# Kernel optimization log

Measured on AMD Instinct MI355X. Metric: run time of the kernel, lower is better.

The kernel has to match this reference:

```python
import jax, jax.numpy as jnp
import numpy as np

B, T, I, H, C, L = 64, 256, 256, 1024, 1000, 2


def setup_inputs() -> dict:
    key = jax.random.key(0)
    ks = jax.random.split(key, 10)
    stdv = 1.0 / np.sqrt(H)
    u = lambda k, shape: jax.random.uniform(k, shape, jnp.float32, -stdv, stdv)
    return {
        "x": jax.random.normal(ks[0], (B, T, I), jnp.float32),
        # gate order: g (tanh), i, f, o — stacked on leading axis
        "W0x": u(ks[1], (4, I, H)),
        "W0h": u(ks[2], (4, H, H)),
        "b0": u(ks[3], (4, H)),
        "W1x": u(ks[4], (4, H, H)),
        "W1h": u(ks[5], (4, H, H)),
        "b1": u(ks[6], (4, H)),
        "Wo": u(ks[7], (H, C)),
        "bo": u(ks[8], (C,)),
    }


def _cell(x, h, c, Wx, Wh, b):
    # z: [4, B, H] — one fused contraction for the 4 gates
    z = jnp.einsum('bi,gih->gbh', x, Wx) + jnp.einsum('bh,ghk->gbk', h, Wh) + b[:, None, :]
    g = jnp.tanh(z[0])
    i = jax.nn.sigmoid(z[1])
    f = jax.nn.sigmoid(z[2])
    o = jax.nn.sigmoid(z[3])
    c_new = g * i + c * f
    h_new = jnp.tanh(c_new) * o
    return h_new, c_new


def reference(x, W0x, W0h, b0, W1x, W1h, b1, Wo, bo):
    xt = jnp.transpose(x, (1, 0, 2))  # [T, B, I] like x.permute(1,0,2)
    zeros = jnp.zeros((B, H), x.dtype)
    init = (zeros, zeros, zeros, zeros)  # h0, c0, h1, c1

    def step(carry, x_t):
        h0, c0, h1, c1 = carry
        h0, c0 = _cell(x_t, h0, c0, W0x, W0h, b0)
        h1, c1 = _cell(h0, h1, c1, W1x, W1h, b1)
        return (h0, c0, h1, c1), None

    (h0, c0, h1, c1), _ = jax.lax.scan(step, init, xt)
    return jnp.matmul(h1, Wo) + bo
```

## Files before the change

kernel.cpp:

```cpp
#include <hip/hip_runtime.h>
#include <cstddef>

#define B_  64
#define T_  256
#define I_  256
#define H_  1024
#define C_  1000
#define BH_ (B_ * H_)
#define SLOTS_B_ 24

typedef _Float16 f16;
typedef __attribute__((ext_vector_type(8))) _Float16 f16x8;
typedef __attribute__((ext_vector_type(4))) float f32x4;

__device__ __forceinline__ float sigmoid_(float v) { return 1.0f / (1.0f + __expf(-v)); }
__device__ __forceinline__ float tanh_(float v) {
  float e = __expf(-2.0f * fabsf(v));
  float t = (1.0f - e) / (1.0f + e);
  return copysignf(t, v);
}

__device__ __forceinline__ void storeH2(f16* p, float a, float b) {
  union { f16 h[2]; unsigned u; } pk;
  pk.h[0] = (f16)a; pk.h[1] = (f16)b;
  __hip_atomic_store((unsigned*)p, pk.u, __ATOMIC_RELAXED, __HIP_MEMORY_SCOPE_AGENT);
}


__device__ __forceinline__ unsigned ldS(unsigned* p) {
  return __hip_atomic_load(p, __ATOMIC_RELAXED, __HIP_MEMORY_SCOPE_AGENT);
}

__device__ __forceinline__ void waitRel(unsigned* a, unsigned ta,
                                        unsigned* b, unsigned tb) {
  int g = 0;
  for (;;) {
    unsigned va = ldS(a);
    unsigned vb = ldS(b);
    if (va >= ta && vb >= tb) break;
    __builtin_amdgcn_s_sleep(1);
    if (++g > (1 << 17)) break;
  }
}

template<bool IS_L1>
__device__ __forceinline__ void role_main(
    const f16* __restrict__ x16,
    const float* __restrict__ Wx, const float* __restrict__ Wh,
    const float* __restrict__ bias,
    f16* __restrict__ h0hist, f16* __restrict__ h1hist,
    unsigned* sync, int bid, int nslots, int fmask, int lagD,
    float* zbAll, float* cLDS, float* biasLDS)
{
  constexpr int KTOT = IS_L1 ? 64 : 40;
  constexpr int NKT  = KTOT / 4;
  constexpr int KX   = IS_L1 ? 1024 : 256;

  const int tid  = threadIdx.x;
  const int wv   = tid >> 6;
  const int nh   = wv >> 2;
  const int kq   = wv & 3;
  const int lane = tid & 63;
  const int c16  = lane & 15;
  const int quad = lane >> 4;
  const int rr7  = bid & 127;
  const int mgroup  = rr7 & 1;
  const int ubase   = (rr7 >> 1) * 16;
  const int rowbase = mgroup * 32;

  const int  grp       = bid & 7;
  const bool leaderBlk = IS_L1 ? (bid == 128) : (bid == 0);
  unsigned* arrBase = sync + (IS_L1 ?  8 :  0) * 32;
  unsigned* relBase = sync + (IS_L1 ? 24 : 16) * 32;
  unsigned* arrMine = arrBase + grp * 32;
  unsigned* relOwn  = relBase + grp * 32;
  unsigned* relOth  = sync + (IS_L1 ? 16 : 24) * 32 + grp * 32;

  if (tid < 64) biasLDS[tid] = bias[(size_t)(tid >> 4) * H_ + ubase + (tid & 15)];
  cLDS[tid] = 0.0f;

  f16x8 Wreg[2][NKT];
  {
    f16* zpan = (f16*)zbAll + wv * 1024;
#pragma unroll
    for (int ii = 0; ii < NKT; ++ii) {
      const int kt = kq * NKT + ii;
#pragma unroll
      for (int rw = 0; rw < 16; ++rw) {
        const int krow  = rw * 2 + (lane >> 5);
        const int col32 = lane & 31;
        const int g = nh * 2 + (col32 >> 4);
        const int u = col32 & 15;
        const int k = kt * 32 + krow;
        float wval = (k < KX) ? Wx[((size_t)g * KX + k) * H_ + ubase + u]
                              : Wh[((size_t)g * H_ + (k - KX)) * H_ + ubase + u];
        zpan[krow * 32 + col32] = (f16)wval;
      }
#pragma unroll
      for (int nt = 0; nt < 2; ++nt) {
        f16x8 f;
#pragma unroll
        for (int j = 0; j < 8; ++j)
          f[j] = zpan[(quad * 8 + j) * 32 + nt * 16 + c16];
        Wreg[nt][ii] = f;
      }
    }
  }
  __syncthreads();

  const int ktbase = kq * NKT;
  const int row0 = rowbase + c16;

#pragma unroll 1
  for (int p = 0; p <= T_; ++p) {
    const bool active = IS_L1 ? (p >= 1) : (p < T_);
    const int do_fence = (nslots == 2) ? 1
                        : ((fmask < 0) ? 0 : (((p & fmask) == fmask) ? 1 : 0));

    if (tid == 0) {
      unsigned  tb = 0u;
      unsigned* bp = relOwn;
      if (IS_L1) {
        if (active) { bp = relOth; tb = (unsigned)p; }
      } else if (active && lagD >= 0 && p > lagD) {
        bp = relOth; tb = (unsigned)(p - lagD);
      }
      waitRel(relOwn, (unsigned)p, bp, tb);
      if (do_fence) __builtin_amdgcn_fence(__ATOMIC_ACQUIRE, "agent");
    }
    __syncthreads();

    if (active) {
      const int sp  = p % nslots;
      const int spm = (p - 1 + nslots) % nslots;
      const int spp = (p + 1) % nslots;
      const f16* __restrict__ hA = h0hist + (size_t)sp * BH_;
      const f16* __restrict__ hB = h1hist + (size_t)spm * BH_;
      f16* __restrict__ hdst = IS_L1 ? (h1hist + (size_t)sp  * BH_)
                                     : (h0hist + (size_t)spp * BH_);

      f16x8 Abuf[6][2];
      auto loadA = [&](int ii, int slot) {
        const int kt = ktbase + ii;
        const int k  = kt * 32 + quad * 8;
#pragma unroll
        for (int mt2 = 0; mt2 < 2; ++mt2) {
          const int row = row0 + mt2 * 16;
          if (!IS_L1 && k < 256) {
            Abuf[slot][mt2] = *(const f16x8*)(x16 + ((size_t)row * T_ + p) * I_ + k);
          } else if (IS_L1 && k >= 1024) {
            Abuf[slot][mt2] = *(const f16x8*)(hB + (size_t)row * H_ + (k - 1024));
          } else {
            const int kk = IS_L1 ? k : (k - 256);
            Abuf[slot][mt2] = *(const f16x8*)(hA + (size_t)row * H_ + kk);
          }
        }
      };

      f32x4 acc[2][2];
#pragma unroll
      for (int mt2 = 0; mt2 < 2; ++mt2)
#pragma unroll
        for (int nt = 0; nt < 2; ++nt)
          acc[mt2][nt] = (f32x4)0.0f;

      loadA(0, 0); loadA(1, 1); loadA(2, 2);
      loadA(3, 3); loadA(4, 4); loadA(5, 5);
#pragma unroll
      for (int i = 0; i < NKT; ++i) {
        const int sl = i % 6;
        const f16x8 a0 = Abuf[sl][0];
        const f16x8 a1 = Abuf[sl][1];
        if (i + 6 < NKT) loadA(i + 6, (i + 6) % 6);
        acc[0][0] = __builtin_amdgcn_mfma_f32_16x16x32_f16(a0, Wreg[0][i], acc[0][0], 0, 0, 0);
        acc[0][1] = __builtin_amdgcn_mfma_f32_16x16x32_f16(a0, Wreg[1][i], acc[0][1], 0, 0, 0);
        acc[1][0] = __builtin_amdgcn_mfma_f32_16x16x32_f16(a1, Wreg[0][i], acc[1][0], 0, 0, 0);
        acc[1][1] = __builtin_amdgcn_mfma_f32_16x16x32_f16(a1, Wreg[1][i], acc[1][1], 0, 0, 0);
      }

      float* zw = zbAll + (nh * 4 + kq) * 1024;
#pragma unroll
      for (int mt2 = 0; mt2 < 2; ++mt2)
#pragma unroll
        for (int nt = 0; nt < 2; ++nt)
#pragma unroll
          for (int e = 0; e < 4; ++e)
            zw[(mt2 * 2 + nt) * 256 + (quad * 4 + e) * 16 + c16] = acc[mt2][nt][e];

      __syncthreads();

      {
        const int base = tid * 4;
        const int nh1  = base >> 10;
        const int off  = base & 1023;
        f32x4 s = (f32x4)0.0f;
#pragma unroll
        for (int q = 0; q < 4; ++q)
          s += *(const f32x4*)(zbAll + nh1 * 4096 + q * 1024 + off);
        const int nt1 = (off >> 8) & 1;
        const int c0  = off & 15;
        s += *(const f32x4*)(biasLDS + (nh1 * 2 + nt1) * 16 + c0);
        *(f32x4*)(zbAll + nh1 * 4096 + off) = s;
      }
      __syncthreads();

      {
        const int row = tid >> 4, u = tid & 15;
        const int mt2 = row >> 4, r16 = row & 15;
        const float z0 = zbAll[0 * 4096 + (mt2 * 2 + 0) * 256 + r16 * 16 + u];
        const float z1 = zbAll[0 * 4096 + (mt2 * 2 + 1) * 256 + r16 * 16 + u];
        const float z2 = zbAll[1 * 4096 + (mt2 * 2 + 0) * 256 + r16 * 16 + u];
        const float z3 = zbAll[1 * 4096 + (mt2 * 2 + 1) * 256 + r16 * 16 + u];
        const float cv = cLDS[tid];
        const float gt = tanh_(z0);
        const float iv = sigmoid_(z1);
        const float fv = sigmoid_(z2);
        const float ov = sigmoid_(z3);
        const float cn = gt * iv + cv * fv;
        cLDS[tid] = cn;
        const float hn = tanh_(cn) * ov;
        const float hn_hi = __shfl_down(hn, 1);
        if ((tid & 1) == 0)
          storeH2(hdst + (size_t)(rowbase + row) * H_ + ubase + u, hn, hn_hi);
      }
    }

    __syncthreads();
    if (tid == 0) {
      __hip_atomic_fetch_add(arrMine, 1u, __ATOMIC_RELAXED, __HIP_MEMORY_SCOPE_AGENT);
      if (leaderBlk) {
        const unsigned tgt = 16u * (unsigned)(p + 1);
        int gg = 0;
        for (;;) {
          unsigned mn = 0xffffffffu;
#pragma unroll
          for (int j = 0; j < 8; ++j) {
            unsigned v = ldS(arrBase + j * 32);
            mn = (v < mn) ? v : mn;
          }
          if (mn >= tgt) break;
          __builtin_amdgcn_s_sleep(1);
          if (++gg > (1 << 17)) break;
        }
#pragma unroll
        for (int j = 0; j < 8; ++j)
          __hip_atomic_store(relBase + j * 32, (unsigned)(p + 1),
                             __ATOMIC_RELAXED, __HIP_MEMORY_SCOPE_AGENT);
      }
    }
  }
}

__global__ __launch_bounds__(512, 2)
void lstm_persistent(const f16* __restrict__ x16,
                     const float* __restrict__ W0x, const float* __restrict__ W0h, const float* __restrict__ b0,
                     const float* __restrict__ W1x, const float* __restrict__ W1h, const float* __restrict__ b1,
                     f16* h0hist, f16* h1hist, unsigned* sync,
                     int nslots, int fmask, int lagD)
{
  __shared__ float zbAll[8192];
  __shared__ float cLDS[512];
  __shared__ float biasLDS[64];
  const int bid = blockIdx.x;
  if (bid >= 128)
    role_main<true >(x16, W1x, W1h, b1, h0hist, h1hist, sync, bid, nslots, fmask, lagD, zbAll, cLDS, biasLDS);
  else
    role_main<false>(x16, W0x, W0h, b0, h0hist, h1hist, sync, bid, nslots, fmask, lagD, zbAll, cLDS, biasLDS);
}

__global__ void cvt_x(const float* __restrict__ xin, f16* __restrict__ xo)
{
  const int i = (blockIdx.x * 256 + threadIdx.x) * 8;
  const float4 a = *(const float4*)(xin + i);
  const float4 b = *(const float4*)(xin + i + 4);
  f16x8 v;
  v[0] = (f16)a.x; v[1] = (f16)a.y; v[2] = (f16)a.z; v[3] = (f16)a.w;
  v[4] = (f16)b.x; v[5] = (f16)b.y; v[6] = (f16)b.z; v[7] = (f16)b.w;
  *(f16x8*)(xo + i) = v;
}

__global__ void out_gemm(const f16* __restrict__ h1,
                         const float* __restrict__ Wo, const float* __restrict__ bo,
                         float* __restrict__ out)
{
  __shared__ float ht[1024][8];
  const int tid = threadIdx.x;
  const int b0r = blockIdx.y * 4;
  for (int i = tid; i < 4096; i += 128) {
    const int rr = i >> 10, k = i & 1023;
    ht[k][rr] = (float)h1[(size_t)(b0r + rr) * H_ + k];
  }
  __syncthreads();
  const int c = blockIdx.x * 125 + tid;
  if (tid < 125) {
    float a0 = 0.f, a1 = 0.f, a2 = 0.f, a3 = 0.f;
#pragma unroll 4
    for (int k = 0; k < 1024; ++k) {
      const float w = Wo[(size_t)k * C_ + c];
      a0 += ht[k][0] * w;
      a1 += ht[k][1] * w;
      a2 += ht[k][2] * w;
      a3 += ht[k][3] * w;
    }
    const float bb = bo[c];
    out[(size_t)(b0r + 0) * C_ + c] = a0 + bb;
    out[(size_t)(b0r + 1) * C_ + c] = a1 + bb;
    out[(size_t)(b0r + 2) * C_ + c] = a2 + bb;
    out[(size_t)(b0r + 3) * C_ + c] = a3 + bb;
  }
}

extern "C" void kernel_launch(void* const* d_in, const int* in_sizes, int n_in,
                              void* d_out, int out_size, void* d_ws, size_t ws_size,
                              hipStream_t stream)
{
  const float* x   = (const float*)d_in[0];
  const float* W0x = (const float*)d_in[1];
  const float* W0h = (const float*)d_in[2];
  const float* b0  = (const float*)d_in[3];
  const float* W1x = (const float*)d_in[4];
  const float* W1h = (const float*)d_in[5];
  const float* b1  = (const float*)d_in[6];
  const float* Wo  = (const float*)d_in[7];
  const float* bo  = (const float*)d_in[8];

  const size_t slotB = (size_t)BH_ * sizeof(f16);
  const size_t xB    = (size_t)B_ * T_ * I_ * sizeof(f16);
  const size_t needA = 4096 + (size_t)2 * (T_ + 1) * slotB + xB;
  const size_t needB = 4096 + (size_t)2 * SLOTS_B_ * slotB + xB;
  int nslots, fmask, lagD;
  if (ws_size >= needA)      { nslots = T_ + 1;   fmask = -1; lagD = -1; }
  else if (ws_size >= needB) { nslots = SLOTS_B_; fmask = 15; lagD = 7;  }
  else                       { nslots = 2;        fmask = 0;  lagD = 0;  }
  const size_t histB = (size_t)nslots * slotB;

  unsigned* sync  = (unsigned*)d_ws;
  f16* h0hist = (f16*)((char*)d_ws + 4096);
  f16* h1hist = (f16*)((char*)h0hist + histB);
  f16* x16    = (f16*)((char*)h1hist + histB);

  hipMemsetAsync(d_ws, 0, 4096 + slotB, stream);
  hipMemsetAsync(h1hist, 0, slotB, stream);

  hipLaunchKernelGGL(cvt_x, dim3((B_ * T_ * I_) / (256 * 8)), dim3(256), 0, stream, x, x16);

  hipLaunchKernelGGL(lstm_persistent, dim3(256), dim3(512), 0, stream,
                     x16, W0x, W0h, b0, W1x, W1h, b1, h0hist, h1hist, sync,
                     nslots, fmask, lagD);

  f16* h1fin = h1hist + (size_t)(T_ % nslots) * BH_;
  hipLaunchKernelGGL(out_gemm, dim3(8, 16), dim3(128), 0, stream,
                     h1fin, Wo, bo, (float*)d_out);
}
```

Measured before the change: 2.980 ms.

## Replace leader-based barrier with per-batch-half counters and overlap waits with x/h compute

Drops the two-stage arrive/leader/release barrier. Each block now polls eight distributed arrival counters directly, partitioned by layer and batch half (mgroup), so it waits only on the blocks that produce the rows it reads. The K-tiles are remapped so each wave has independent work before each wait: layer 0 computes its x-projection tiles and layer 1 its h0 tiles before waiting on the other dependency. This aims to cut barrier latency and hide part of it behind MFMA work. In exchange, every block spins on eight counters, which adds polling traffic, and correctness now depends on the new counter-slot and indexing scheme.

```diff
diff --git a/kernel.cpp b/kernel.cpp
--- a/kernel.cpp
+++ b/kernel.cpp
@@ -31,13 +31,16 @@
   return __hip_atomic_load(p, __ATOMIC_RELAXED, __HIP_MEMORY_SCOPE_AGENT);
 }
 
-__device__ __forceinline__ void waitRel(unsigned* a, unsigned ta,
-                                        unsigned* b, unsigned tb) {
+__device__ __forceinline__ void waitCtr8(unsigned* base, unsigned tgt) {
   int g = 0;
   for (;;) {
-    unsigned va = ldS(a);
-    unsigned vb = ldS(b);
-    if (va >= ta && vb >= tb) break;
+    unsigned mn = 0xffffffffu;
+#pragma unroll
+    for (int j = 0; j < 8; ++j) {
+      unsigned v = ldS(base + j * 32);
+      mn = (v < mn) ? v : mn;
+    }
+    if (mn >= tgt) break;
     __builtin_amdgcn_s_sleep(1);
     if (++g > (1 << 17)) break;
   }
@@ -52,9 +55,8 @@
     unsigned* sync, int bid, int nslots, int fmask, int lagD,
     float* zbAll, float* cLDS, float* biasLDS)
 {
-  constexpr int KTOT = IS_L1 ? 64 : 40;
-  constexpr int NKT  = KTOT / 4;
-  constexpr int KX   = IS_L1 ? 1024 : 256;
+  constexpr int NKT = IS_L1 ? 16 : 10;
+  constexpr int KX  = IS_L1 ? 1024 : 256;
 
   const int tid  = threadIdx.x;
   const int wv   = tid >> 6;
@@ -68,13 +70,16 @@
   const int ubase   = (rr7 >> 1) * 16;
   const int rowbase = mgroup * 32;
 
-  const int  grp       = bid & 7;
-  const bool leaderBlk = IS_L1 ? (bid == 128) : (bid == 0);
-  unsigned* arrBase = sync + (IS_L1 ?  8 :  0) * 32;
-  unsigned* relBase = sync + (IS_L1 ? 24 : 16) * 32;
-  unsigned* arrMine = arrBase + grp * 32;
-  unsigned* relOwn  = relBase + grp * 32;
-  unsigned* relOth  = sync + (IS_L1 ? 16 : 24) * 32 + grp * 32;
+  const int sub = (rr7 >> 1) & 7;
+  unsigned* ctrC0 = sync + ((0 * 2 + mgroup) * 8) * 32;
+  unsigned* ctrC1 = sync + ((1 * 2 + mgroup) * 8) * 32;
+  unsigned* ctrOwn = IS_L1 ? ctrC1 : ctrC0;
+  unsigned* arrLine = ctrOwn + sub * 32;
+
+  auto kmap = [&](int ii) -> int {
+    if (!IS_L1) return (ii < 2) ? (kq * 2 + ii) * 32 : 256 + (kq * 8 + (ii - 2)) * 32;
+    else        return (ii < 8) ? (kq * 8 + ii) * 32 : 1024 + (kq * 8 + (ii - 8)) * 32;
+  };
 
   if (tid < 64) biasLDS[tid] = bias[(size_t)(tid >> 4) * H_ + ubase + (tid & 15)];
   cLDS[tid] = 0.0f;
@@ -84,14 +89,14 @@
     f16* zpan = (f16*)zbAll + wv * 1024;
 #pragma unroll
     for (int ii = 0; ii < NKT; ++ii) {
-      const int kt = kq * NKT + ii;
+      const int kbase = kmap(ii);
 #pragma unroll
       for (int rw = 0; rw < 16; ++rw) {
         const int krow  = rw * 2 + (lane >> 5);
         const int col32 = lane & 31;
         const int g = nh * 2 + (col32 >> 4);
         const int u = col32 & 15;
-        const int k = kt * 32 + krow;
+        const int k = kbase + krow;
         float wval = (k < KX) ? Wx[((size_t)g * KX + k) * H_ + ubase + u]
                               : Wh[((size_t)g * H_ + (k - KX)) * H_ + ubase + u];
         zpan[krow * 32 + col32] = (f16)wval;
@@ -108,7 +113,6 @@
   }
   __syncthreads();
 
-  const int ktbase = kq * NKT;
   const int row0 = rowbase + c16;
 
 #pragma unroll 1
@@ -116,19 +120,6 @@
     const bool active = IS_L1 ? (p >= 1) : (p < T_);
     const int do_fence = (nslots == 2) ? 1
                         : ((fmask < 0) ? 0 : (((p & fmask) == fmask) ? 1 : 0));
-
-    if (tid == 0) {
-      unsigned  tb = 0u;
-      unsigned* bp = relOwn;
-      if (IS_L1) {
-        if (active) { bp = relOth; tb = (unsigned)p; }
-      } else if (active && lagD >= 0 && p > lagD) {
-        bp = relOth; tb = (unsigned)(p - lagD);
-      }
-      waitRel(relOwn, (unsigned)p, bp, tb);
-      if (do_fence) __builtin_amdgcn_fence(__ATOMIC_ACQUIRE, "agent");
-    }
-    __syncthreads();
 
     if (active) {
       const int sp  = p % nslots;
@@ -139,21 +130,21 @@
       f16* __restrict__ hdst = IS_L1 ? (h1hist + (size_t)sp  * BH_)
                                      : (h0hist + (size_t)spp * BH_);
 
-      f16x8 Abuf[6][2];
-      auto loadA = [&](int ii, int slot) {
-        const int kt = ktbase + ii;
-        const int k  = kt * 32 + quad * 8;
+      f16x8 Abuf[8][2];
+      auto loadTile = [&](int ii, int slot) {
+        const int kb = kmap(ii) + quad * 8;
 #pragma unroll
         for (int mt2 = 0; mt2 < 2; ++mt2) {
           const int row = row0 + mt2 * 16;
-          if (!IS_L1 && k < 256) {
-            Abuf[slot][mt2] = *(const f16x8*)(x16 + ((size_t)row * T_ + p) * I_ + k);
-          } else if (IS_L1 && k >= 1024) {
-            Abuf[slot][mt2] = *(const f16x8*)(hB + (size_t)row * H_ + (k - 1024));
+          const f16* src;
+          if (!IS_L1) {
+            src = (ii < 2) ? (x16 + ((size_t)row * T_ + p) * I_ + kb)
+                           : (hA + (size_t)row * H_ + (kb - 256));
           } else {
-            const int kk = IS_L1 ? k : (k - 256);
-            Abuf[slot][mt2] = *(const f16x8*)(hA + (size_t)row * H_ + kk);
+            src = (ii < 8) ? (hA + (size_t)row * H_ + kb)
+                           : (hB + (size_t)row * H_ + (kb - 1024));
           }
+          Abuf[slot][mt2] = *(const f16x8*)src;
         }
       };
 
@@ -164,18 +155,47 @@
         for (int nt = 0; nt < 2; ++nt)
           acc[mt2][nt] = (f32x4)0.0f;
 
-      loadA(0, 0); loadA(1, 1); loadA(2, 2);
-      loadA(3, 3); loadA(4, 4); loadA(5, 5);
-#pragma unroll
-      for (int i = 0; i < NKT; ++i) {
-        const int sl = i % 6;
-        const f16x8 a0 = Abuf[sl][0];
-        const f16x8 a1 = Abuf[sl][1];
-        if (i + 6 < NKT) loadA(i + 6, (i + 6) % 6);
-        acc[0][0] = __builtin_amdgcn_mfma_f32_16x16x32_f16(a0, Wreg[0][i], acc[0][0], 0, 0, 0);
-        acc[0][1] = __builtin_amdgcn_mfma_f32_16x16x32_f16(a0, Wreg[1][i], acc[0][1], 0, 0, 0);
-        acc[1][0] = __builtin_amdgcn_mfma_f32_16x16x32_f16(a1, Wreg[0][i], acc[1][0], 0, 0, 0);
-        acc[1][1] = __builtin_amdgcn_mfma_f32_16x16x32_f16(a1, Wreg[1][i], acc[1][1], 0, 0, 0);
+      auto mfma4 = [&](int slot, int ii) {
+        const f16x8 a0 = Abuf[slot][0];
+        const f16x8 a1 = Abuf[slot][1];
+        acc[0][0] = __builtin_amdgcn_mfma_f32_16x16x32_f16(a0, Wreg[0][ii], acc[0][0], 0, 0, 0);
+        acc[0][1] = __builtin_amdgcn_mfma_f32_16x16x32_f16(a0, Wreg[1][ii], acc[0][1], 0, 0, 0);
+        acc[1][0] = __builtin_amdgcn_mfma_f32_16x16x32_f16(a1, Wreg[0][ii], acc[1][0], 0, 0, 0);
+        acc[1][1] = __builtin_amdgcn_mfma_f32_16x16x32_f16(a1, Wreg[1][ii], acc[1][1], 0, 0, 0);
+      };
+
+      if (!IS_L1) {
+        loadTile(0, 0); loadTile(1, 1);
+        mfma4(0, 0); mfma4(1, 1);
+        if (tid == 0) {
+          waitCtr8(ctrC0, 8u * (unsigned)p);
+          if (lagD >= 0 && p > lagD) waitCtr8(ctrC1, 8u * (unsigned)(p - lagD));
+          if (do_fence) __builtin_amdgcn_fence(__ATOMIC_ACQUIRE, "agent");
+        }
+        __syncthreads();
+#pragma unroll
+        for (int ii = 2; ii < 10; ++ii) loadTile(ii, ii - 2);
+#pragma unroll
+        for (int ii = 2; ii < 10; ++ii) mfma4(ii - 2, ii);
+      } else {
+        if (tid == 0) {
+          waitCtr8(ctrC0, 8u * (unsigned)p);
+          if (do_fence) __builtin_amdgcn_fence(__ATOMIC_ACQUIRE, "agent");
+        }
+        __syncthreads();
+#pragma unroll
+        for (int ii = 0; ii < 8; ++ii) loadTile(ii, ii);
+#pragma unroll
+        for (int ii = 0; ii < 8; ++ii) mfma4(ii, ii);
+        if (tid == 0) {
+          waitCtr8(ctrC1, 8u * (unsigned)p);
+          if (do_fence) __builtin_amdgcn_fence(__ATOMIC_ACQUIRE, "agent");
+        }
+        __syncthreads();
+#pragma unroll
+        for (int ii = 8; ii < 16; ++ii) loadTile(ii, ii - 8);
+#pragma unroll
+        for (int ii = 8; ii < 16; ++ii) mfma4(ii - 8, ii);
       }
 
       float* zw = zbAll + (nh * 4 + kq) * 1024;
@@ -226,28 +246,8 @@
     }
 
     __syncthreads();
-    if (tid == 0) {
-      __hip_atomic_fetch_add(arrMine, 1u, __ATOMIC_RELAXED, __HIP_MEMORY_SCOPE_AGENT);
-      if (leaderBlk) {
-        const unsigned tgt = 16u * (unsigned)(p + 1);
-        int gg = 0;
-        for (;;) {
-          unsigned mn = 0xffffffffu;
-#pragma unroll
-          for (int j = 0; j < 8; ++j) {
-            unsigned v = ldS(arrBase + j * 32);
-            mn = (v < mn) ? v : mn;
-          }
-          if (mn >= tgt) break;
-          __builtin_amdgcn_s_sleep(1);
-          if (++gg > (1 << 17)) break;
-        }
-#pragma unroll
-        for (int j = 0; j < 8; ++j)
-          __hip_atomic_store(relBase + j * 32, (unsigned)(p + 1),
-                             __ATOMIC_RELAXED, __HIP_MEMORY_SCOPE_AGENT);
-      }
-    }
+    if (tid == 0)
+      __hip_atomic_fetch_add(arrLine, 1u, __ATOMIC_RELAXED, __HIP_MEMORY_SCOPE_AGENT);
   }
 }
 
```

Result: faster. 2.542 ms (-14.7%).
